# Kernel optimization log

Measured on AMD Instinct MI355X. Metric: run time of the kernel, lower is better.

Reference implementation:

```python
import jax, jax.numpy as jnp
import numpy as np

L, S, B, E, H, FF = 512, 2048, 4, 1024, 16, 2048
HD = E // H  # 64


def _layernorm(x, g, b, eps=1e-5):
    m = jnp.mean(x, axis=-1, keepdims=True)
    v = jnp.mean((x - m) ** 2, axis=-1, keepdims=True)
    return (x - m) * jax.lax.rsqrt(v + eps) * g + b


def _decoder(tgt, memory, pos, query_pos,
             in_proj_w, in_proj_b, out_w, out_b,
             cq_w, cq_b, ck_w, ck_b, cv_w, cv_b,
             down_w, down_b, lin1_w, lin1_b, lin2_w, lin2_b,
             n1_g, n1_b, n2_g, n2_b, n3_g, n3_b):
    Lq, Bb, Em = tgt.shape
    scale = 1.0 / np.sqrt(HD).astype(np.float32)
    # --- self attention (torch nn.MultiheadAttention, eval mode, no masks) ---
    qk_in = tgt + query_pos
    Wq, Wk, Wv = jnp.split(in_proj_w, 3, axis=0)
    bq, bk, bv = jnp.split(in_proj_b, 3)
    q = (qk_in @ Wq.T + bq).reshape(Lq, Bb, H, HD)
    k = (qk_in @ Wk.T + bk).reshape(Lq, Bb, H, HD)
    v = (tgt @ Wv.T + bv).reshape(Lq, Bb, H, HD)
    attn = jax.nn.softmax(jnp.einsum('lbhd,mbhd->bhlm', q, k) * scale, axis=-1)
    ctx = jnp.einsum('bhlm,mbhd->lbhd', attn, v).reshape(Lq, Bb, Em)
    tgt = _layernorm(tgt + ctx @ out_w.T + out_b, n1_g, n1_b)
    # --- custom cross attention; inputs permuted to [B, E, N] (Conv1d k=1 == matmul) ---
    qc = jnp.einsum('oe,lbe->bol', cq_w, tgt + query_pos) + cq_b[None, :, None]
    kc = jnp.einsum('oe,sbe->bos', ck_w, memory + pos) + ck_b[None, :, None]
    vc = jnp.einsum('oe,sbe->bos', cv_w, memory) + cv_b[None, :, None]
    # view(B, head_dim, num_heads, N): channel axis splits as (HD, H)
    qc = qc.reshape(Bb, HD, H, -1)
    kc = kc.reshape(Bb, HD, H, -1)
    vc = vc.reshape(Bb, HD, H, -1)
    # scores_2[b,d,h,m] = kc[b,d,h,m] * sum_{d',n} qc[b,d',h,n] kc[b,d',h,m] / sqrt(HD)
    # (einsum('abcd,aced->abcd', key, scores_1) broadcasts key over the summed n axis)
    s1sum = jnp.einsum('bdh,bdhm->bhm', qc.sum(-1), kc) * scale
    prob = jax.nn.softmax(kc * s1sum[:, None, :, :], axis=-1)        # [B,HD,H,S]
    o = jnp.einsum('bnhm,bdhm->bdhn', prob, vc)                       # [B,HD,H,HD]
    o = (o @ down_w.T + down_b).reshape(Bb, Em, 1)                    # Linear HD->1, then view
    tgt = _layernorm(tgt + jnp.transpose(o, (2, 0, 1)), n2_g, n2_b)   # [1,B,E] broadcasts over L
    # --- FFN ---
    ff = jax.nn.relu(tgt @ lin1_w.T + lin1_b) @ lin2_w.T + lin2_b
    return _layernorm(tgt + ff, n3_g, n3_b)


def setup_inputs() -> dict:
    key = jax.random.key(0)
    ks = jax.random.split(key, 16)
    def nrm(k, shape, s=0.02):
        return (s * jax.random.normal(k, shape)).astype(jnp.float32)
    z = lambda *s: jnp.zeros(s, jnp.float32)
    return dict(
        tgt=nrm(ks[0], (L, B, E), 1.0),
        memory=nrm(ks[1], (S, B, E), 1.0),
        pos=nrm(ks[2], (S, B, E), 1.0),
        query_pos=nrm(ks[3], (L, B, E), 1.0),
        in_proj_w=nrm(ks[4], (3 * E, E)), in_proj_b=z(3 * E),
        out_w=nrm(ks[5], (E, E)), out_b=z(E),
        cq_w=nrm(ks[6], (E, E)), cq_b=z(E),
        ck_w=nrm(ks[7], (E, E)), ck_b=z(E),
        cv_w=nrm(ks[8], (E, E)), cv_b=z(E),
        down_w=nrm(ks[9], (1, HD)), down_b=z(1),
        lin1_w=nrm(ks[10], (FF, E)), lin1_b=z(FF),
        lin2_w=nrm(ks[11], (E, FF)), lin2_b=z(E),
        n1_g=jnp.ones((E,), jnp.float32), n1_b=z(E),
        n2_g=jnp.ones((E,), jnp.float32), n2_b=z(E),
        n3_g=jnp.ones((E,), jnp.float32), n3_b=z(E),
    )


def reference(tgt, memory, pos, query_pos,
              in_proj_w, in_proj_b, out_w, out_b,
              cq_w, cq_b, ck_w, ck_b, cv_w, cv_b,
              down_w, down_b, lin1_w, lin1_b, lin2_w, lin2_b,
              n1_g, n1_b, n2_g, n2_b, n3_g, n3_b):
    return _decoder(tgt, memory, pos, query_pos,
                    in_proj_w, in_proj_b, out_w, out_b,
                    cq_w, cq_b, ck_w, ck_b, cv_w, cv_b,
                    down_w, down_b, lin1_w, lin1_b, lin2_w, lin2_b,
                    n1_g, n1_b, n2_g, n2_b, n3_g, n3_b)
```

## Files before the change

### kernel.cpp

```cpp
#include <hip/hip_runtime.h>
#include <hip/hip_bf16.h>

typedef __hip_bfloat16 bf16;
typedef short short8 __attribute__((ext_vector_type(8)));
typedef float f32x4 __attribute__((ext_vector_type(4)));

#define Lq 512
#define Sm 2048
#define Bb 4
#define Ee 1024
#define Hh 16
#define FFd 2048
#define HDd 64

static __device__ __forceinline__ float b2f(bf16 x) { return __bfloat162float(x); }
static __device__ __forceinline__ bf16 f2b(float x) { return __float2bfloat16(x); }
static __device__ __forceinline__ unsigned short bits(bf16 x) {
    return __builtin_bit_cast(unsigned short, x);
}
static __device__ __forceinline__ float us2f(unsigned short u) {
    return b2f(__builtin_bit_cast(bf16, u));
}

static __device__ __forceinline__ void gload16(const void* g, void* l) {
    __builtin_amdgcn_global_load_lds(
        (const __attribute__((address_space(1))) unsigned int*)g,
        (__attribute__((address_space(3))) unsigned int*)l, 16, 0, 0);
}

__global__ __launch_bounds__(512, 2)
void kcvc_gemm(const bf16* __restrict__ wk, const bf16* __restrict__ wv,
               const bf16* __restrict__ mp, const bf16* __restrict__ mo,
               bf16* __restrict__ kc, bf16* __restrict__ vc,
               const float* __restrict__ kb, const float* __restrict__ vb)
{
    constexpr int BK = 64;
    __shared__ bf16 lA[2][256 * BK];
    __shared__ bf16 lB[2][256 * BK];

    const int tid  = threadIdx.x;
    const int lane = tid & 63;
    const int wm = (tid >> 6) >> 2;
    const int wn = (tid >> 6) & 3;

    int bid = (blockIdx.x & 7) * 32 + (blockIdx.x >> 3);
    const int bx = bid & 3;
    const int by = (bid >> 2) & 7;
    const int z  = bid >> 5;

    const bool isv = z >= 4;
    const int  b   = isv ? z - 4 : z;
    const bf16*  A    = isv ? wv : wk;
    const bf16*  B    = (isv ? mo : mp) + b * 1024;
    bf16*        C    = (isv ? vc : kc) + (long)b * 2097152;
    const float* bias = isv ? vb : kb;

    const int m0 = bx * 256, n0 = by * 256;
    const bf16* Abase = A + (long)m0 * 1024;
    const bf16* Bbase = B + (long)n0 * 4096;

    const int kgrp = lane >> 4, l16 = lane & 15;
    const int rsw = l16 & 7;

    auto stage = [&](int buf, int k0) {
#pragma unroll
        for (int r = 0; r < 4; r++) {
            int c = r * 512 + tid;
            int row = c >> 3;
            int ss = (c & 7) ^ (row & 7);
            gload16(Abase + (long)row * 1024 + k0 + ss * 8, &lA[buf][c * 8]);
        }
#pragma unroll
        for (int r = 0; r < 4; r++) {
            int c = r * 512 + tid;
            int row = c >> 3;
            int ss = (c & 7) ^ (row & 7);
            gload16(Bbase + (long)row * 4096 + k0 + ss * 8, &lB[buf][c * 8]);
        }
    };

    f32x4 acc[8][4];
#pragma unroll
    for (int i = 0; i < 8; i++)
#pragma unroll
        for (int j = 0; j < 4; j++) acc[i][j] = f32x4{0.f, 0.f, 0.f, 0.f};

    stage(0, 0);
    asm volatile("s_waitcnt vmcnt(0)" ::: "memory");
    __builtin_amdgcn_s_barrier();

    constexpr int NT = 16;
    for (int t = 0; t < NT; t++) {
        if (t + 1 < NT) stage((t + 1) & 1, (t + 1) * BK);

        const bf16* la = lA[t & 1];
        const bf16* lb = lB[t & 1];
#pragma unroll
        for (int h = 0; h < 2; h++) {
            const int sd = ((h * 4 + kgrp) ^ rsw) * 8;
            short8 af[8], bv[4];
#pragma unroll
            for (int i = 0; i < 8; i++)
                af[i] = *(const short8*)&la[(wm * 128 + i * 16 + l16) * BK + sd];
#pragma unroll
            for (int j = 0; j < 4; j++)
                bv[j] = *(const short8*)&lb[(wn * 64 + j * 16 + l16) * BK + sd];
            __builtin_amdgcn_s_setprio(1);
#pragma unroll
            for (int i = 0; i < 8; i++)
#pragma unroll
                for (int j = 0; j < 4; j++)
                    acc[i][j] = __builtin_amdgcn_mfma_f32_16x16x32_bf16(af[i], bv[j], acc[i][j], 0, 0, 0);
            __builtin_amdgcn_s_setprio(0);
        }

        asm volatile("s_waitcnt vmcnt(0)" ::: "memory");
        __builtin_amdgcn_s_barrier();
    }

#pragma unroll
    for (int i = 0; i < 8; i++) {
#pragma unroll
        for (int j = 0; j < 4; j++) {
#pragma unroll
            for (int r = 0; r < 4; r++) {
                int row = m0 + wm * 128 + i * 16 + kgrp * 4 + r;
                int col = n0 + wn * 64 + j * 16 + l16;
                float v = acc[i][j][r] + bias[row];
                float v2 = __shfl_xor(v, 1);
                if (!(l16 & 1)) {
                    unsigned int pk = (unsigned int)bits(f2b(v)) |
                                      ((unsigned int)bits(f2b(v2)) << 16);
                    *(unsigned int*)&C[(long)row * 2048 + col] = pk;
                }
            }
        }
    }
}

__global__ __launch_bounds__(512, 2)
void flash_attn(const bf16* __restrict__ qk, const bf16* __restrict__ vt,
                bf16* __restrict__ ctx)
{
    __shared__ bf16 lQ[128 * 64];
    __shared__ bf16 lK[2][64 * 64];
    __shared__ bf16 lV[2][64 * 64];
    __shared__ bf16 lP[128 * 64];
    __shared__ float scb[128];

    const int tid  = threadIdx.x;
    const int lane = tid & 63;
    const int wq   = tid >> 6;
    const int kgrp = lane >> 4, l16 = lane & 15;

    const int qt = blockIdx.x & 3;
    const int bh = blockIdx.x >> 2;
    const int b = bh >> 4, h = bh & 15;
    const int L0 = qt * 128;

#pragma unroll
    for (int it = 0; it < 2; it++) {
        int c = it * 512 + tid;
        int rr = c >> 3, sl = c & 7, ss = sl ^ (rr & 7);
        gload16(qk + ((long)(L0 + rr) * 4 + b) * 2048 + h * 64 + ss * 8,
                &lQ[(it * 512 + wq * 64) * 8]);
    }

    auto stageKV = [&](int buf, int st) {
        int rr = tid >> 3, sl = tid & 7, ss = sl ^ (rr & 7);
        gload16(qk + ((long)(st * 64 + rr) * 4 + b) * 2048 + 1024 + h * 64 + ss * 8,
                &lK[buf][(wq * 64) * 8]);
        gload16(vt + ((long)(b * 1024 + h * 64 + rr)) * 512 + st * 64 + ss * 8,
                &lV[buf][(wq * 64) * 8]);
    };

    auto frag = [&](const bf16* base, int row, int kk) {
        return *(const short8*)&base[row * 64 + (((kk * 4 + kgrp) ^ (l16 & 7)) * 8)];
    };

    f32x4 acc_o[4];
#pragma unroll
    for (int j = 0; j < 4; j++) acc_o[j] = f32x4{0.f, 0.f, 0.f, 0.f};
    float m_run = -1e30f, l_run = 0.f;

    stageKV(0, 0);
    asm volatile("s_waitcnt vmcnt(0)" ::: "memory");
    __builtin_amdgcn_s_barrier();

    int buf = 0;
    for (int st = 0; st < 8; st++) {
        if (st < 7) stageKV(buf ^ 1, st + 1);

        f32x4 accs[4];
#pragma unroll
        for (int fm = 0; fm < 4; fm++) accs[fm] = f32x4{0.f, 0.f, 0.f, 0.f};
        __builtin_amdgcn_s_setprio(1);
#pragma unroll
        for (int kk = 0; kk < 2; kk++) {
            short8 bq = frag(lQ, wq * 16 + l16, kk);
#pragma unroll
            for (int fm = 0; fm < 4; fm++) {
                short8 af = frag(lK[buf], fm * 16 + l16, kk);
                accs[fm] = __builtin_amdgcn_mfma_f32_16x16x32_bf16(af, bq, accs[fm], 0, 0, 0);
            }
        }
        __builtin_amdgcn_s_setprio(0);

        float v[4][4], p[4][4];
        float tmax = -1e30f;
#pragma unroll
        for (int fm = 0; fm < 4; fm++)
#pragma unroll
            for (int r = 0; r < 4; r++) {
                v[fm][r] = accs[fm][r] * 0.125f;
                tmax = fmaxf(tmax, v[fm][r]);
            }
        tmax = fmaxf(tmax, __shfl_xor(tmax, 16));
        tmax = fmaxf(tmax, __shfl_xor(tmax, 32));
        float m_new = fmaxf(m_run, tmax);
        float sc = __expf(m_run - m_new);
        float sum = 0.f;
#pragma unroll
        for (int fm = 0; fm < 4; fm++)
#pragma unroll
            for (int r = 0; r < 4; r++) {
                p[fm][r] = __expf(v[fm][r] - m_new);
                sum += p[fm][r];
            }
        sum += __shfl_xor(sum, 16);
        sum += __shfl_xor(sum, 32);
        l_run = l_run * sc + sum;
        m_run = m_new;

        if (!kgrp) scb[wq * 16 + l16] = sc;
        asm volatile("s_waitcnt lgkmcnt(0)" ::: "memory");
        __builtin_amdgcn_sched_barrier(0);
        float sc2[4];
#pragma unroll
        for (int r = 0; r < 4; r++) sc2[r] = scb[wq * 16 + kgrp * 4 + r];
#pragma unroll
        for (int fn = 0; fn < 4; fn++)
#pragma unroll
            for (int r = 0; r < 4; r++) acc_o[fn][r] *= sc2[r];

#pragma unroll
        for (int fm = 0; fm < 4; fm++) {
            int l = wq * 16 + l16;
            int sp = (fm * 2 + (kgrp >> 1)) ^ (l16 & 7);
            uint2 pk;
            pk.x = (unsigned int)bits(f2b(p[fm][0])) | ((unsigned int)bits(f2b(p[fm][1])) << 16);
            pk.y = (unsigned int)bits(f2b(p[fm][2])) | ((unsigned int)bits(f2b(p[fm][3])) << 16);
            *(uint2*)&lP[l * 64 + sp * 8 + (kgrp & 1) * 4] = pk;
        }
        asm volatile("s_waitcnt lgkmcnt(0)" ::: "memory");
        __builtin_amdgcn_sched_barrier(0);

        __builtin_amdgcn_s_setprio(1);
#pragma unroll
        for (int kk = 0; kk < 2; kk++) {
            short8 ap = frag(lP, wq * 16 + l16, kk);
#pragma unroll
            for (int fn = 0; fn < 4; fn++) {
                short8 bvf = frag(lV[buf], fn * 16 + l16, kk);
                acc_o[fn] = __builtin_amdgcn_mfma_f32_16x16x32_bf16(ap, bvf, acc_o[fn], 0, 0, 0);
            }
        }
        __builtin_amdgcn_s_setprio(0);

        asm volatile("s_waitcnt vmcnt(0)" ::: "memory");
        __builtin_amdgcn_s_barrier();
        buf ^= 1;
    }

    if (!kgrp) scb[wq * 16 + l16] = 1.f / l_run;
    asm volatile("s_waitcnt lgkmcnt(0)" ::: "memory");
    __builtin_amdgcn_sched_barrier(0);
    float inv[4];
#pragma unroll
    for (int r = 0; r < 4; r++) inv[r] = scb[wq * 16 + kgrp * 4 + r];
#pragma unroll
    for (int fn = 0; fn < 4; fn++) {
#pragma unroll
        for (int r = 0; r < 4; r++) {
            int lg = L0 + wq * 16 + kgrp * 4 + r;
            int d  = fn * 16 + l16;
            float vv = acc_o[fn][r] * inv[r];
            float v2 = __shfl_xor(vv, 1);
            if (!(l16 & 1)) {
                unsigned int pk = (unsigned int)bits(f2b(vv)) |
                                  ((unsigned int)bits(f2b(v2)) << 16);
                *(unsigned int*)&ctx[((long)lg * 4 + b) * 1024 + h * 64 + d] = pk;
            }
        }
    }
}

template<int BM, int BN>
__global__ __launch_bounds__(256)
void gemm_nt(const bf16* __restrict__ A, const bf16* __restrict__ Bw,
             float* __restrict__ Cf, bf16* __restrict__ Cb,
             const float* __restrict__ bias,
             const bf16* __restrict__ A2, const bf16* __restrict__ B2,
             bf16* __restrict__ Cb2, const float* __restrict__ bias2,
             int gx, int gy,
             int K, long lda, long ldb, long ldc,
             long sA1, long sA2, long sB1, long sB2, long sC1, long sC2,
             int zdiv, int zsplit, int nsplit, float alpha, int mode, int mode2)
{
    constexpr int BK = 64;
    constexpr int RA = BM / 32, RB = BN / 32;
    __shared__ bf16 lA[2][BM * BK];
    __shared__ bf16 lB[2][BN * BK];

    const int tid  = threadIdx.x;
    const int lane = tid & 63;
    const int wave = tid >> 6;
    const int wm = wave >> 1, wn = wave & 1;
    constexpr int RM = BM / 2, RN = BN / 2;
    constexpr int FM = RM / 16, FN = RN / 16;

    const int nwg = gridDim.x;
    const int cpx = nwg >> 3;
    int bid = (blockIdx.x & 7) * cpx + (blockIdx.x >> 3);
    const int bx = bid % gx;
    int tmp = bid / gx;
    const int by = tmp % gy;
    const int z  = tmp / gy;

    const int m0 = bx * BM;
    const int n0 = by * BN;

    const bool use2 = (z >= zsplit) || (n0 >= nsplit);
    const int  zz   = (z >= zsplit) ? z - zsplit : z;
    const bf16*  Ap = (use2 && A2)    ? A2    : A;
    const bf16*  Bp = (use2 && B2)    ? B2    : Bw;
    const float* bp = (use2 && bias2) ? bias2 : bias;
    const int    md = use2 ? mode2 : mode;
    bf16*        Co = (use2 && Cb2)   ? Cb2   : Cb;

    const long offA = (long)(zz / zdiv) * sA1 + (long)(zz % zdiv) * sA2;
    const long offB = (long)(zz / zdiv) * sB1 + (long)(zz % zdiv) * sB2;
    const long offC = (long)(zz / zdiv) * sC1 + (long)(zz % zdiv) * sC2;

    const bf16* Abase = Ap + offA + (long)m0 * lda;
    const bf16* Bbase = Bp + offB + (long)n0 * ldb;

    const int kgrp = lane >> 4;
    const int l16  = lane & 15;
    const int rsw  = l16 & 7;

    auto stage = [&](int buf, int k0) {
#pragma unroll
        for (int r = 0; r < RA; r++) {
            int c = r * 256 + tid;
            int row = c >> 3;
            int ss = (c & 7) ^ (row & 7);
            gload16(Abase + (long)row * lda + k0 + ss * 8, &lA[buf][c * 8]);
        }
#pragma unroll
        for (int r = 0; r < RB; r++) {
            int c = r * 256 + tid;
            int row = c >> 3;
            int ss = (c & 7) ^ (row & 7);
            gload16(Bbase + (long)row * ldb + k0 + ss * 8, &lB[buf][c * 8]);
        }
    };

    f32x4 acc[FM][FN];
#pragma unroll
    for (int i = 0; i < FM; i++)
#pragma unroll
        for (int j = 0; j < FN; j++) acc[i][j] = f32x4{0.f, 0.f, 0.f, 0.f};

    const int nt = K / BK;
    stage(0, 0);
    asm volatile("s_waitcnt vmcnt(0)" ::: "memory");
    __builtin_amdgcn_s_barrier();

    for (int t = 0; t < nt; t++) {
        if (t + 1 < nt) stage((t + 1) & 1, (t + 1) * BK);

        const bf16* la = lA[t & 1];
        const bf16* lb = lB[t & 1];
#pragma unroll
        for (int h = 0; h < 2; h++) {
            const int sd = ((h * 4 + kgrp) ^ rsw) * 8;
            short8 af[FM], bv[FN];
#pragma unroll
            for (int i = 0; i < FM; i++)
                af[i] = *(const short8*)&la[(wm * RM + i * 16 + l16) * BK + sd];
#pragma unroll
            for (int j = 0; j < FN; j++)
                bv[j] = *(const short8*)&lb[(wn * RN + j * 16 + l16) * BK + sd];
            __builtin_amdgcn_s_setprio(1);
#pragma unroll
            for (int i = 0; i < FM; i++)
#pragma unroll
                for (int j = 0; j < FN; j++)
                    acc[i][j] = __builtin_amdgcn_mfma_f32_16x16x32_bf16(af[i], bv[j], acc[i][j], 0, 0, 0);
            __builtin_amdgcn_s_setprio(0);
        }

        asm volatile("s_waitcnt vmcnt(0)" ::: "memory");
        __builtin_amdgcn_s_barrier();
    }

#pragma unroll
    for (int i = 0; i < FM; i++) {
#pragma unroll
        for (int j = 0; j < FN; j++) {
#pragma unroll
            for (int r = 0; r < 4; r++) {
                int row = m0 + wm * RM + i * 16 + kgrp * 4 + r;
                int col = n0 + wn * RN + j * 16 + l16;
                float v = alpha * acc[i][j][r] + (bp ? bp[col] : 0.f);
                float v2 = __shfl_xor(v, 1);
                if (md == 0) {
                    if (!(l16 & 1)) {
                        float2 pv = {v, v2};
                        *(float2*)&Cf[offC + (long)row * ldc + col] = pv;
                    }
                } else if (md == 1) {
                    if (!(l16 & 1)) {
                        unsigned int pk = (unsigned int)bits(f2b(v)) |
                                          ((unsigned int)bits(f2b(v2)) << 16);
                        *(unsigned int*)&Co[offC + (long)row * ldc + col] = pk;
                    }
                } else if (md == 2) {
                    if (!(l16 & 1)) {
                        unsigned int pk = (unsigned int)bits(f2b(fmaxf(v, 0.f))) |
                                          ((unsigned int)bits(f2b(fmaxf(v2, 0.f))) << 16);
                        *(unsigned int*)&Co[offC + (long)row * ldc + col] = pk;
                    }
                } else {
                    int o = col - nsplit;
                    Cb2[((long)(row & 3) * 1024 + o) * 512 + (row >> 2)] = f2b(v);
                }
            }
        }
    }
}

struct Cvt2Seg { const float* a; const float* b; bf16* d; bf16* d2; int nblk; };
struct Cvt2Args { Cvt2Seg s[8]; };

__global__ __launch_bounds__(256)
void cvt_kernel(Cvt2Args args)
{
    for (int ci = blockIdx.x; ci < 10240; ci += 2048) {
        int rem = ci;
        int si = 0;
        while (si < 7 && rem >= args.s[si].nblk) { rem -= args.s[si].nblk; si++; }
        Cvt2Seg sg = args.s[si];
        const long i = (long)rem * 2048 + threadIdx.x * 8;

        float4 a0 = *(const float4*)(sg.a + i);
        float4 a1 = *(const float4*)(sg.a + i + 4);
        float4 s0 = a0, s1 = a1;
        if (sg.b) {
            float4 b0 = *(const float4*)(sg.b + i);
            float4 b1 = *(const float4*)(sg.b + i + 4);
            s0.x += b0.x; s0.y += b0.y; s0.z += b0.z; s0.w += b0.w;
            s1.x += b1.x; s1.y += b1.y; s1.z += b1.z; s1.w += b1.w;
        }
        short8 u;
        u[0] = (short)bits(f2b(s0.x)); u[1] = (short)bits(f2b(s0.y));
        u[2] = (short)bits(f2b(s0.z)); u[3] = (short)bits(f2b(s0.w));
        u[4] = (short)bits(f2b(s1.x)); u[5] = (short)bits(f2b(s1.y));
        u[6] = (short)bits(f2b(s1.z)); u[7] = (short)bits(f2b(s1.w));
        *(short8*)((unsigned short*)sg.d + i) = u;
        if (sg.d2) {
            short8 w;
            w[0] = (short)bits(f2b(a0.x)); w[1] = (short)bits(f2b(a0.y));
            w[2] = (short)bits(f2b(a0.z)); w[3] = (short)bits(f2b(a0.w));
            w[4] = (short)bits(f2b(a1.x)); w[5] = (short)bits(f2b(a1.y));
            w[6] = (short)bits(f2b(a1.z)); w[7] = (short)bits(f2b(a1.w));
            *(short8*)((unsigned short*)sg.d2 + i) = w;
        }
    }
}

__global__ __launch_bounds__(256)
void ln_kernel(const float* __restrict__ x, const bf16* __restrict__ xB,
               const float* __restrict__ res, const float* __restrict__ resb,
               const float* __restrict__ g, const float* __restrict__ be,
               float* __restrict__ outF, bf16* __restrict__ outB)
{
    long row = blockIdx.x;
    int tid = threadIdx.x, lane = tid & 63, w = tid >> 6;
    float vv[4];
    if (x) {
        float4 xv = *(const float4*)(x + row * 1024 + tid * 4);
        vv[0] = xv.x; vv[1] = xv.y; vv[2] = xv.z; vv[3] = xv.w;
    } else {
        ushort4 xv = *(const ushort4*)((const unsigned short*)xB + row * 1024 + tid * 4);
        vv[0] = us2f(xv.x); vv[1] = us2f(xv.y); vv[2] = us2f(xv.z); vv[3] = us2f(xv.w);
    }
    if (res) {
        float4 rv = *(const float4*)(res + row * 1024 + tid * 4);
        vv[0] += rv.x; vv[1] += rv.y; vv[2] += rv.z; vv[3] += rv.w;
    }
    if (resb) {
        float4 rv = *(const float4*)(resb + (row & 3) * 1024 + tid * 4);
        vv[0] += rv.x; vv[1] += rv.y; vv[2] += rv.z; vv[3] += rv.w;
    }
    float s = vv[0] + vv[1] + vv[2] + vv[3];
    float q = vv[0] * vv[0] + vv[1] * vv[1] + vv[2] * vv[2] + vv[3] * vv[3];
    __shared__ float rs[4], rq[4];
    for (int o = 32; o; o >>= 1) { s += __shfl_xor(s, o); q += __shfl_xor(q, o); }
    if (!lane) { rs[w] = s; rq[w] = q; }
    __syncthreads();
    s = rs[0] + rs[1] + rs[2] + rs[3];
    q = rq[0] + rq[1] + rq[2] + rq[3];
    float mean = s * (1.f / 1024.f);
    float var  = q * (1.f / 1024.f) - mean * mean;
    float rstd = rsqrtf(var + 1e-5f);
    float4 gv = *(const float4*)(g + tid * 4);
    float4 bv = *(const float4*)(be + tid * 4);
    float o0 = (vv[0] - mean) * rstd * gv.x + bv.x;
    float o1 = (vv[1] - mean) * rstd * gv.y + bv.y;
    float o2 = (vv[2] - mean) * rstd * gv.z + bv.z;
    float o3 = (vv[3] - mean) * rstd * gv.w + bv.w;
    if (outF) {
        float4 ov = {o0, o1, o2, o3};
        *(float4*)(outF + row * 1024 + tid * 4) = ov;
    }
    if (outB) {
        ushort4 u;
        u.x = bits(f2b(o0)); u.y = bits(f2b(o1));
        u.z = bits(f2b(o2)); u.w = bits(f2b(o3));
        *reinterpret_cast<ushort4*>((unsigned short*)outB + row * 1024 + tid * 4) = u;
    }
}

__global__ __launch_bounds__(256)
void asum_part_kernel(const float* __restrict__ t1, const float* __restrict__ qp,
                      float* __restrict__ part)
{
    int blk = blockIdx.x;
    int lc = blk >> 4, b = (blk >> 2) & 3, ec = blk & 3;
    int e = ec * 256 + threadIdx.x;
    float acc = 0.f;
#pragma unroll 4
    for (int l = lc * 32; l < lc * 32 + 32; l++) {
        long idx = ((long)(l * 4 + b)) * 1024 + e;
        acc += t1[idx] + qp[idx];
    }
    part[(lc * 4 + b) * 1024 + e] = acc;
}

__global__ __launch_bounds__(256)
void asum_reduce_kernel(const float* __restrict__ part, float* __restrict__ asum)
{
    int b = blockIdx.x >> 2, ec = blockIdx.x & 3;
    int e = ec * 256 + threadIdx.x;
    float acc = 0.f;
#pragma unroll
    for (int lc = 0; lc < 16; lc++) acc += part[(lc * 4 + b) * 1024 + e];
    asum[b * 1024 + e] = acc;
}

__global__ __launch_bounds__(256)
void qsum_kernel(const float* __restrict__ cqw, const float* __restrict__ cqb,
                 const float* __restrict__ asum, float* __restrict__ qsum)
{
    int o = blockIdx.x * 4 + (threadIdx.x >> 6);
    int lane = threadIdx.x & 63;
    float a0 = 0, a1 = 0, a2 = 0, a3 = 0;
    for (int j = 0; j < 16; j++) {
        int e = lane + j * 64;
        float wv = cqw[(long)o * 1024 + e];
        a0 += wv * asum[e];
        a1 += wv * asum[1024 + e];
        a2 += wv * asum[2048 + e];
        a3 += wv * asum[3072 + e];
    }
    for (int t = 32; t; t >>= 1) {
        a0 += __shfl_xor(a0, t); a1 += __shfl_xor(a1, t);
        a2 += __shfl_xor(a2, t); a3 += __shfl_xor(a3, t);
    }
    if (!lane) {
        float bb = 512.f * cqb[o];
        qsum[o] = a0 + bb; qsum[1024 + o] = a1 + bb;
        qsum[2048 + o] = a2 + bb; qsum[3072 + o] = a3 + bb;
    }
}

__global__ __launch_bounds__(256)
void s1_kernel(const bf16* __restrict__ kc, const float* __restrict__ qsum,
               float* __restrict__ s1)
{
    int bh = blockIdx.x, b = bh >> 4, h = bh & 15;
    int m = blockIdx.y * 256 + threadIdx.x;
    __shared__ float qd[64];
    if (threadIdx.x < 64) qd[threadIdx.x] = qsum[b * 1024 + threadIdx.x * 16 + h];
    __syncthreads();
    const bf16* kcb = kc + (long)b * 2048 * 1024 + (long)h * 2048 + m;
    float acc = 0.f;
#pragma unroll 8
    for (int d = 0; d < 64; d++) acc += qd[d] * b2f(kcb[(long)d * 16 * 2048]);
    s1[(long)bh * 2048 + m] = acc * 0.125f;
}

__global__ __launch_bounds__(256)
void bsum_kernel(const bf16* __restrict__ kc, const float* __restrict__ s1,
                 float* __restrict__ rmax, float* __restrict__ rsum)
{
    int bh = blockIdx.x >> 6, n = blockIdx.x & 63;
    int b = bh >> 4, h = bh & 15;
    int tid = threadIdx.x, lane = tid & 63, w = tid >> 6;
    const bf16* row = kc + (long)b * 2048 * 1024 + (long)(n * 16 + h) * 2048;
    const float* s1r = s1 + (long)bh * 2048;
    float t[8];
    float mx = -1e30f;
#pragma unroll
    for (int i = 0; i < 8; i++) {
        int m = tid + i * 256;
        t[i] = b2f(row[m]) * s1r[m];
        mx = fmaxf(mx, t[i]);
    }
    __shared__ float redm[4], reds[4];
    for (int o = 32; o; o >>= 1) mx = fmaxf(mx, __shfl_xor(mx, o));
    if (!lane) redm[w] = mx;
    __syncthreads();
    mx = fmaxf(fmaxf(redm[0], redm[1]), fmaxf(redm[2], redm[3]));
    float s = 0.f;
#pragma unroll
    for (int i = 0; i < 8; i++) s += __expf(t[i] - mx);
    for (int o = 32; o; o >>= 1) s += __shfl_xor(s, o);
    if (!lane) reds[w] = s;
    __syncthreads();
    if (!tid) {
        rmax[bh * 64 + n] = mx;
        rsum[bh * 64 + n] = reds[0] + reds[1] + reds[2] + reds[3];
    }
}

__global__ __launch_bounds__(256)
void wpr_kernel(const bf16* __restrict__ kc, const float* __restrict__ s1,
                const float* __restrict__ rmax, const float* __restrict__ rsum,
                const float* __restrict__ dw, float* __restrict__ wpr)
{
    int bh = blockIdx.x, b = bh >> 4, h = bh & 15;
    int m = blockIdx.y * 256 + threadIdx.x;
    __shared__ float cf[64], cm[64];
    if (threadIdx.x < 64) {
        cf[threadIdx.x] = dw[threadIdx.x] / rsum[bh * 64 + threadIdx.x];
        cm[threadIdx.x] = rmax[bh * 64 + threadIdx.x];
    }
    __syncthreads();
    float s1v = s1[(long)bh * 2048 + m];
    const bf16* kcb = kc + (long)b * 2048 * 1024 + (long)h * 2048 + m;
    float acc = 0.f;
#pragma unroll 8
    for (int n = 0; n < 64; n++)
        acc += cf[n] * __expf(b2f(kcb[(long)n * 16 * 2048]) * s1v - cm[n]);
    wpr[(long)bh * 2048 + m] = acc;
}

__global__ __launch_bounds__(256)
void cout_kernel(const bf16* __restrict__ vc, const float* __restrict__ wpr,
                 const float* __restrict__ db, float* __restrict__ outs)
{
    int bh = blockIdx.x >> 2, dg = blockIdx.x & 3;
    int b = bh >> 4, h = bh & 15;
    int tid = threadIdx.x, lane = tid & 63, w = tid >> 6;
    __shared__ float lwpr[2048];
#pragma unroll
    for (int i = 0; i < 8; i++) lwpr[tid + i * 256] = wpr[(long)bh * 2048 + tid + i * 256];
    __syncthreads();
#pragma unroll
    for (int dd = 0; dd < 4; dd++) {
        int d = dg * 16 + w * 4 + dd;
        int o = d * 16 + h;
        const bf16* vrow = vc + (long)b * 2048 * 1024 + (long)o * 2048;
        float acc = 0.f;
#pragma unroll
        for (int j = 0; j < 4; j++) {
            int m = j * 512 + lane * 8;
            short8 vv = *(const short8*)&vrow[m];
#pragma unroll
            for (int k = 0; k < 8; k++) {
                bf16 bb = __builtin_bit_cast(bf16, (unsigned short)vv[k]);
                acc += lwpr[m + k] * b2f(bb);
            }
        }
        for (int t2 = 32; t2; t2 >>= 1) acc += __shfl_xor(acc, t2);
        if (!lane) outs[b * 1024 + o] = acc + db[0];
    }
}

extern "C" void kernel_launch(void* const* d_in, const int* in_sizes, int n_in,
                              void* d_out, int out_size, void* d_ws, size_t ws_size,
                              hipStream_t stream)
{
    const float* tgt  = (const float*)d_in[0];
    const float* mem  = (const float*)d_in[1];
    const float* pos  = (const float*)d_in[2];
    const float* qp   = (const float*)d_in[3];
    const float* ipw  = (const float*)d_in[4];
    const float* ipb  = (const float*)d_in[5];
    const float* outw = (const float*)d_in[6];
    const float* outb = (const float*)d_in[7];
    const float* cqw  = (const float*)d_in[8];
    const float* cqb  = (const float*)d_in[9];
    const float* ckw  = (const float*)d_in[10];
    const float* ckb  = (const float*)d_in[11];
    const float* cvw  = (const float*)d_in[12];
    const float* cvb  = (const float*)d_in[13];
    const float* dww  = (const float*)d_in[14];
    const float* dwb  = (const float*)d_in[15];
    const float* l1w  = (const float*)d_in[16];
    const float* l1b  = (const float*)d_in[17];
    const float* l2w  = (const float*)d_in[18];
    const float* l2b  = (const float*)d_in[19];
    const float* n1g  = (const float*)d_in[20];
    const float* n1b  = (const float*)d_in[21];
    const float* n2g  = (const float*)d_in[22];
    const float* n2b  = (const float*)d_in[23];
    const float* n3g  = (const float*)d_in[24];
    const float* n3b  = (const float*)d_in[25];

    char* ws = (char*)d_ws;
    auto MB = [](long x) { return x << 20; };
    bf16* w_ip    = (bf16*)(ws + MB(0));
    bf16* w_out   = (bf16*)(ws + MB(6));
    bf16* w_ck    = (bf16*)(ws + MB(8));
    bf16* w_cv    = (bf16*)(ws + MB(10));
    bf16* w_l1    = (bf16*)(ws + MB(12));
    bf16* w_l2    = (bf16*)(ws + MB(16));
    bf16* qkin    = (bf16*)(ws + MB(20));
    bf16* tgtb    = (bf16*)(ws + MB(24));
    bf16* memposb = (bf16*)(ws + MB(28));
    bf16* memb    = (bf16*)(ws + MB(44));
    bf16* qkbuf   = (bf16*)(ws + MB(60));
    bf16* vtb     = (bf16*)(ws + MB(68));
    bf16* kcb     = (bf16*)(ws + MB(72));
    bf16* ctxb    = (bf16*)(ws + MB(104));
    bf16* atmpb   = (bf16*)(ws + MB(108));
    float* s1buf  = (float*)(ws + MB(108));
    float* wprbuf = (float*)(ws + MB(109));
    float* rmax   = (float*)(ws + MB(110));
    float* rsum   = (float*)(ws + MB(110) + (64 << 10));
    float* part   = (float*)(ws + MB(111));
    float* tgt1   = (float*)(ws + MB(116));
    float* asum   = (float*)(ws + MB(124));
    float* qsum   = (float*)(ws + MB(125));
    bf16* vcb     = (bf16*)(ws + MB(126));
    float* outs   = (float*)(ws + MB(142));
    float* tgt2   = (float*)(ws + MB(143));
    bf16* tgt2b   = (bf16*)(ws + MB(151));
    bf16* ff1b    = (bf16*)(ws + MB(155));
    bf16* ff2b    = (bf16*)(ws + MB(163));

    const int BIGZ = 1000000, BIGN = 1 << 30;

    Cvt2Args ca{};
    ca.s[0] = {ipw,  nullptr, w_ip,    nullptr, 1536};
    ca.s[1] = {outw, nullptr, w_out,   nullptr, 512};
    ca.s[2] = {ckw,  nullptr, w_ck,    nullptr, 512};
    ca.s[3] = {cvw,  nullptr, w_cv,    nullptr, 512};
    ca.s[4] = {l1w,  nullptr, w_l1,    nullptr, 1024};
    ca.s[5] = {l2w,  nullptr, w_l2,    nullptr, 1024};
    ca.s[6] = {tgt,  qp,      qkin,    tgtb,    1024};
    ca.s[7] = {mem,  pos,     memposb, memb,    4096};
    cvt_kernel<<<dim3(2048, 1, 1), 256, 0, stream>>>(ca);

    gemm_nt<64, 128><<<dim3(768, 1, 1), 256, 0, stream>>>(
        qkin, w_ip, nullptr, qkbuf, ipb,
        tgtb, nullptr, vtb, nullptr,
        32, 24,
        1024, 1024, 1024, 2048,
        0, 0, 0, 0, 0, 0, 1, BIGZ, 2048, 1.f, 1, 3);

    flash_attn<<<dim3(256, 1, 1), 512, 0, stream>>>(qkbuf, vtb, ctxb);

    gemm_nt<64, 128><<<dim3(256, 1, 1), 256, 0, stream>>>(
        ctxb, w_out, nullptr, atmpb, outb,
        nullptr, nullptr, nullptr, nullptr,
        32, 8,
        1024, 1024, 1024, 1024,
        0, 0, 0, 0, 0, 0, 1, BIGZ, BIGN, 1.f, 1, 1);

    ln_kernel<<<dim3(2048, 1, 1), 256, 0, stream>>>(
        nullptr, atmpb, tgt, nullptr, n1g, n1b, tgt1, nullptr);

    asum_part_kernel<<<dim3(256, 1, 1), 256, 0, stream>>>(tgt1, qp, part);
    asum_reduce_kernel<<<dim3(16, 1, 1), 256, 0, stream>>>(part, asum);
    qsum_kernel<<<dim3(256, 1, 1), 256, 0, stream>>>(cqw, cqb, asum, qsum);

    kcvc_gemm<<<dim3(256, 1, 1), 512, 0, stream>>>(
        w_ck, w_cv, memposb, memb, kcb, vcb, ckb, cvb);

    s1_kernel<<<dim3(64, 8, 1), 256, 0, stream>>>(kcb, qsum, s1buf);
    bsum_kernel<<<dim3(4096, 1, 1), 256, 0, stream>>>(kcb, s1buf, rmax, rsum);
    wpr_kernel<<<dim3(64, 8, 1), 256, 0, stream>>>(kcb, s1buf, rmax, rsum, dww, wprbuf);
    cout_kernel<<<dim3(256, 1, 1), 256, 0, stream>>>(vcb, wprbuf, dwb, outs);

    ln_kernel<<<dim3(2048, 1, 1), 256, 0, stream>>>(
        tgt1, nullptr, nullptr, outs, n2g, n2b, tgt2, tgt2b);

    gemm_nt<64, 128><<<dim3(512, 1, 1), 256, 0, stream>>>(
        tgt2b, w_l1, nullptr, ff1b, l1b,
        nullptr, nullptr, nullptr, nullptr,
        32, 16,
        1024, 1024, 1024, 2048,
        0, 0, 0, 0, 0, 0, 1, BIGZ, BIGN, 1.f, 2, 2);

    gemm_nt<64, 128><<<dim3(256, 1, 1), 256, 0, stream>>>(
        ff1b, w_l2, nullptr, ff2b, l2b,
        nullptr, nullptr, nullptr, nullptr,
        32, 8,
        2048, 2048, 2048, 1024,
        0, 0, 0, 0, 0, 0, 1, BIGZ, BIGN, 1.f, 1, 1);

    ln_kernel<<<dim3(2048, 1, 1), 256, 0, stream>>>(
        nullptr, ff2b, tgt2, nullptr, n3g, n3b, (float*)d_out, nullptr);
}
```

Before: 257.8 us.

## Fuse memory+pos fp32-to-bf16 conversion into the K/V projection GEMM loads

The K/V cross-attention GEMM now reads fp32 memory and pos directly, adds them in registers, converts to bf16 and writes the B tile to LDS. This replaces the separate conversion pass and its intermediate bf16 buffers. B loads are software-pipelined in two halves around the MFMA blocks. The aim is to cut the extra HBM round trip of the conversion kernel, at the cost of doubled-width B reads repeated across M tiles and a register-staged load path instead of direct global-to-LDS copies.

```diff
diff --git a/kernel.cpp b/kernel.cpp
--- a/kernel.cpp
+++ b/kernel.cpp
@@ -28,9 +28,18 @@
         (__attribute__((address_space(3))) unsigned int*)l, 16, 0, 0);
 }
 
+static __device__ __forceinline__ short8 pack8(float4 a0, float4 a1) {
+    short8 u;
+    u[0] = (short)bits(f2b(a0.x)); u[1] = (short)bits(f2b(a0.y));
+    u[2] = (short)bits(f2b(a0.z)); u[3] = (short)bits(f2b(a0.w));
+    u[4] = (short)bits(f2b(a1.x)); u[5] = (short)bits(f2b(a1.y));
+    u[6] = (short)bits(f2b(a1.z)); u[7] = (short)bits(f2b(a1.w));
+    return u;
+}
+
 __global__ __launch_bounds__(512, 2)
 void kcvc_gemm(const bf16* __restrict__ wk, const bf16* __restrict__ wv,
-               const bf16* __restrict__ mp, const bf16* __restrict__ mo,
+               const float* __restrict__ mem, const float* __restrict__ pos,
                bf16* __restrict__ kc, bf16* __restrict__ vc,
                const float* __restrict__ kb, const float* __restrict__ vb)
 {
@@ -51,18 +60,18 @@
     const bool isv = z >= 4;
     const int  b   = isv ? z - 4 : z;
     const bf16*  A    = isv ? wv : wk;
-    const bf16*  B    = (isv ? mo : mp) + b * 1024;
     bf16*        C    = (isv ? vc : kc) + (long)b * 2097152;
     const float* bias = isv ? vb : kb;
 
     const int m0 = bx * 256, n0 = by * 256;
-    const bf16* Abase = A + (long)m0 * 1024;
-    const bf16* Bbase = B + (long)n0 * 4096;
+    const bf16*  Abase = A + (long)m0 * 1024;
+    const float* Bm = mem + (long)n0 * 4096 + b * 1024;
+    const float* Bp = pos + (long)n0 * 4096 + b * 1024;
 
     const int kgrp = lane >> 4, l16 = lane & 15;
     const int rsw = l16 & 7;
 
-    auto stage = [&](int buf, int k0) {
+    auto stageA = [&](int buf, int k0) {
 #pragma unroll
         for (int r = 0; r < 4; r++) {
             int c = r * 512 + tid;
@@ -70,14 +79,39 @@
             int ss = (c & 7) ^ (row & 7);
             gload16(Abase + (long)row * 1024 + k0 + ss * 8, &lA[buf][c * 8]);
         }
-#pragma unroll
-        for (int r = 0; r < 4; r++) {
-            int c = r * 512 + tid;
+    };
+
+    float4 bm[2][2], bq[2][2];
+    auto loadB = [&](int hh, int k0) {
+#pragma unroll
+        for (int r = 0; r < 2; r++) {
+            int c = (hh * 2 + r) * 512 + tid;
             int row = c >> 3;
             int ss = (c & 7) ^ (row & 7);
-            gload16(Bbase + (long)row * 4096 + k0 + ss * 8, &lB[buf][c * 8]);
+            const float* s = Bm + (long)row * 4096 + k0 + ss * 8;
+            bm[r][0] = *(const float4*)s;
+            bm[r][1] = *(const float4*)(s + 4);
+            if (!isv) {
+                const float* p = Bp + (long)row * 4096 + k0 + ss * 8;
+                bq[r][0] = *(const float4*)p;
+                bq[r][1] = *(const float4*)(p + 4);
+            }
         }
     };
+    auto writeB = [&](int buf, int hh) {
+#pragma unroll
+        for (int r = 0; r < 2; r++) {
+            int c = (hh * 2 + r) * 512 + tid;
+            float4 a0 = bm[r][0], a1 = bm[r][1];
+            if (!isv) {
+                a0.x += bq[r][0].x; a0.y += bq[r][0].y;
+                a0.z += bq[r][0].z; a0.w += bq[r][0].w;
+                a1.x += bq[r][1].x; a1.y += bq[r][1].y;
+                a1.z += bq[r][1].z; a1.w += bq[r][1].w;
+            }
+            *(short8*)&lB[buf][c * 8] = pack8(a0, a1);
+        }
+    };
 
     f32x4 acc[8][4];
 #pragma unroll
@@ -85,19 +119,26 @@
 #pragma unroll
         for (int j = 0; j < 4; j++) acc[i][j] = f32x4{0.f, 0.f, 0.f, 0.f};
 
-    stage(0, 0);
+    stageA(0, 0);
+    loadB(0, 0);
     asm volatile("s_waitcnt vmcnt(0)" ::: "memory");
+    writeB(0, 0);
+    loadB(1, 0);
+    asm volatile("s_waitcnt vmcnt(0)" ::: "memory");
+    writeB(0, 1);
+    asm volatile("s_waitcnt lgkmcnt(0)" ::: "memory");
     __builtin_amdgcn_s_barrier();
 
     constexpr int NT = 16;
     for (int t = 0; t < NT; t++) {
-        if (t + 1 < NT) stage((t + 1) & 1, (t + 1) * BK);
-
-        const bf16* la = lA[t & 1];
-        const bf16* lb = lB[t & 1];
-#pragma unroll
-        for (int h = 0; h < 2; h++) {
-            const int sd = ((h * 4 + kgrp) ^ rsw) * 8;
+        const int buf = t & 1;
+        const int k1 = (t + 1) * BK;
+        if (t + 1 < NT) { stageA(buf ^ 1, k1); loadB(0, k1); }
+
+        const bf16* la = lA[buf];
+        const bf16* lb = lB[buf];
+        {
+            const int sd = ((0 * 4 + kgrp) ^ rsw) * 8;
             short8 af[8], bv[4];
 #pragma unroll
             for (int i = 0; i < 8; i++)
@@ -113,8 +154,33 @@
                     acc[i][j] = __builtin_amdgcn_mfma_f32_16x16x32_bf16(af[i], bv[j], acc[i][j], 0, 0, 0);
             __builtin_amdgcn_s_setprio(0);
         }
-
-        asm volatile("s_waitcnt vmcnt(0)" ::: "memory");
+        if (t + 1 < NT) {
+            asm volatile("s_waitcnt vmcnt(0)" ::: "memory");
+            writeB(buf ^ 1, 0);
+            loadB(1, k1);
+        }
+        {
+            const int sd = ((1 * 4 + kgrp) ^ rsw) * 8;
+            short8 af[8], bv[4];
+#pragma unroll
+            for (int i = 0; i < 8; i++)
+                af[i] = *(const short8*)&la[(wm * 128 + i * 16 + l16) * BK + sd];
+#pragma unroll
+            for (int j = 0; j < 4; j++)
+                bv[j] = *(const short8*)&lb[(wn * 64 + j * 16 + l16) * BK + sd];
+            __builtin_amdgcn_s_setprio(1);
+#pragma unroll
+            for (int i = 0; i < 8; i++)
+#pragma unroll
+                for (int j = 0; j < 4; j++)
+                    acc[i][j] = __builtin_amdgcn_mfma_f32_16x16x32_bf16(af[i], bv[j], acc[i][j], 0, 0, 0);
+            __builtin_amdgcn_s_setprio(0);
+        }
+        if (t + 1 < NT) {
+            asm volatile("s_waitcnt vmcnt(0)" ::: "memory");
+            writeB(buf ^ 1, 1);
+        }
+        asm volatile("s_waitcnt lgkmcnt(0)" ::: "memory");
         __builtin_amdgcn_s_barrier();
     }
 
@@ -447,7 +513,7 @@
 __global__ __launch_bounds__(256)
 void cvt_kernel(Cvt2Args args)
 {
-    for (int ci = blockIdx.x; ci < 10240; ci += 2048) {
+    for (int ci = blockIdx.x; ci < 6144; ci += 2048) {
         int rem = ci;
         int si = 0;
         while (si < 7 && rem >= args.s[si].nblk) { rem -= args.s[si].nblk; si++; }
@@ -463,19 +529,9 @@
             s0.x += b0.x; s0.y += b0.y; s0.z += b0.z; s0.w += b0.w;
             s1.x += b1.x; s1.y += b1.y; s1.z += b1.z; s1.w += b1.w;
         }
-        short8 u;
-        u[0] = (short)bits(f2b(s0.x)); u[1] = (short)bits(f2b(s0.y));
-        u[2] = (short)bits(f2b(s0.z)); u[3] = (short)bits(f2b(s0.w));
-        u[4] = (short)bits(f2b(s1.x)); u[5] = (short)bits(f2b(s1.y));
-        u[6] = (short)bits(f2b(s1.z)); u[7] = (short)bits(f2b(s1.w));
-        *(short8*)((unsigned short*)sg.d + i) = u;
+        *(short8*)((unsigned short*)sg.d + i) = pack8(s0, s1);
         if (sg.d2) {
-            short8 w;
-            w[0] = (short)bits(f2b(a0.x)); w[1] = (short)bits(f2b(a0.y));
-            w[2] = (short)bits(f2b(a0.z)); w[3] = (short)bits(f2b(a0.w));
-            w[4] = (short)bits(f2b(a1.x)); w[5] = (short)bits(f2b(a1.y));
-            w[6] = (short)bits(f2b(a1.z)); w[7] = (short)bits(f2b(a1.w));
-            *(short8*)((unsigned short*)sg.d2 + i) = w;
+            *(short8*)((unsigned short*)sg.d2 + i) = pack8(a0, a1);
         }
     }
 }
@@ -731,8 +787,6 @@
     bf16* w_l2    = (bf16*)(ws + MB(16));
     bf16* qkin    = (bf16*)(ws + MB(20));
     bf16* tgtb    = (bf16*)(ws + MB(24));
-    bf16* memposb = (bf16*)(ws + MB(28));
-    bf16* memb    = (bf16*)(ws + MB(44));
     bf16* qkbuf   = (bf16*)(ws + MB(60));
     bf16* vtb     = (bf16*)(ws + MB(68));
     bf16* kcb     = (bf16*)(ws + MB(72));
@@ -763,7 +817,6 @@
     ca.s[4] = {l1w,  nullptr, w_l1,    nullptr, 1024};
     ca.s[5] = {l2w,  nullptr, w_l2,    nullptr, 1024};
     ca.s[6] = {tgt,  qp,      qkin,    tgtb,    1024};
-    ca.s[7] = {mem,  pos,     memposb, memb,    4096};
     cvt_kernel<<<dim3(2048, 1, 1), 256, 0, stream>>>(ca);
 
     gemm_nt<64, 128><<<dim3(768, 1, 1), 256, 0, stream>>>(
@@ -790,7 +843,7 @@
     qsum_kernel<<<dim3(256, 1, 1), 256, 0, stream>>>(cqw, cqb, asum, qsum);
 
     kcvc_gemm<<<dim3(256, 1, 1), 512, 0, stream>>>(
-        w_ck, w_cv, memposb, memb, kcb, vcb, ckb, cvb);
+        w_ck, w_cv, mem, pos, kcb, vcb, ckb, cvb);
 
     s1_kernel<<<dim3(64, 8, 1), 256, 0, stream>>>(kcb, qsum, s1buf);
     bsum_kernel<<<dim3(4096, 1, 1), 256, 0, stream>>>(kcb, s1buf, rmax, rsum);
```

After: 260.5 us. About the same (+1.1%).
